# Kernel tuning notes

Measured on AMD Instinct MI355X. Metric: run time of the kernel, lower is better.

Reference implementation:

```python
import jax, jax.numpy as jnp
import numpy as np

B, D, V, T = 256, 1024, 32000, 64  # num_seqs, hidden dim, vocab, history len


def setup_inputs() -> dict:
    key = jax.random.key(0)
    ks = jax.random.split(key, 8)
    hidden = jax.random.normal(ks[0], (B, D), dtype=jnp.float32)
    embedding = jax.random.normal(ks[1], (V, D), dtype=jnp.float32) * (1.0 / np.sqrt(D))
    output_tokens = jax.random.randint(ks[2], (B, T), 0, V, dtype=jnp.int64)
    presence_penalties = jax.random.uniform(ks[3], (B,), dtype=jnp.float32)
    frequency_penalties = jax.random.uniform(ks[4], (B,), dtype=jnp.float32)
    temperatures = jax.random.uniform(ks[5], (B,), dtype=jnp.float32) + 0.5  # > eps
    top_ps = jax.random.uniform(ks[6], (B,), dtype=jnp.float32) * 0.5 + 0.5  # in [0.5, 1.0)
    top_ks = jax.random.randint(ks[7], (B,), 1, V, dtype=jnp.int64)
    return {
        "hidden": hidden,
        "embedding": embedding,
        "output_tokens": output_tokens,
        "presence_penalties": presence_penalties,
        "frequency_penalties": frequency_penalties,
        "temperatures": temperatures,
        "top_ps": top_ps,
        "top_ks": top_ks,
    }


def reference(hidden, embedding, output_tokens, presence_penalties,
              frequency_penalties, temperatures, top_ps, top_ks):
    # 1) logits = pruned hidden states @ embedding^T  -> [B, V]
    logits = jnp.einsum("bd,vd->bv", hidden, embedding)
    b, v = logits.shape

    # 2) presence/frequency penalties via per-row token histogram (np.bincount equiv)
    rows = jnp.broadcast_to(jnp.arange(b)[:, None], output_tokens.shape)
    counts = jnp.zeros((b, v), logits.dtype).at[rows, output_tokens].add(1.0)
    logits = logits - frequency_penalties[:, None] * counts \
                    - presence_penalties[:, None] * (counts > 0).astype(logits.dtype)

    # 3) temperature scaling
    logits = logits / temperatures[:, None]

    # 4) probabilities
    probs = jax.nn.softmax(logits, axis=-1)

    # 5) top-p / top-k: descending sort, cumsum masks, scatter back via inverse perm
    order = jnp.argsort(-probs, axis=-1)                       # descending order
    probs_sort = jnp.take_along_axis(probs, order, axis=-1)
    probs_cum = jnp.cumsum(probs_sort, axis=-1)
    top_p_mask = (probs_cum - probs_sort) > top_ps[:, None]
    top_k_mask = jnp.arange(v)[None, :] >= top_ks[:, None]
    probs_sort = jnp.where(top_p_mask | top_k_mask, 0.0, probs_sort)
    inv = jnp.argsort(order, axis=-1)
    filtered_probs = jnp.take_along_axis(probs_sort, inv, axis=-1)  # original order
    return filtered_probs
```

## Files before the change

### kernel.cpp

```cpp
#include <hip/hip_runtime.h>
#include <math.h>

#define NB 256
#define NV 32000
#define ND 1024
#define NT 64

#define GN 64
#define ASTR 56
#define NKB 64
#define ASLAB (256 * ASTR)
#define NGBLK (NV / GN)
#define INV2048F 4.8828125e-4f

#define NBIN 1024
#define HSTR 1032
#define HTOT (4 * HSTR)
#define FIX2 4294967296.0
#define SMASK ((1ull << 48) - 1ull)
#define SMEM_BYTES (NV * 4 + HTOT * 4)

typedef _Float16 f16x8 __attribute__((ext_vector_type(8)));
typedef _Float16 f16x4 __attribute__((ext_vector_type(4)));
typedef float f32x16 __attribute__((ext_vector_type(16)));
typedef __attribute__((address_space(3))) void lds_void;
typedef __attribute__((address_space(1))) void glb_void;

struct RowP2 {
  unsigned long long basePack;
  unsigned long long toppZfix;
  unsigned pfx;
  int ktop;
  float invZ;
  unsigned ustar;
  int m;
  int cEq;
};

__device__ __forceinline__ unsigned mono_enc(float f) {
  unsigned u = __float_as_uint(f);
  return (u & 0x80000000u) ? ~u : (u | 0x80000000u);
}
__device__ __forceinline__ float mono_dec(unsigned u) {
  return (u & 0x80000000u) ? __uint_as_float(u & 0x7FFFFFFFu) : __uint_as_float(~u);
}

__global__ __launch_bounds__(256) void convert_A(const float* __restrict__ hidden,
                                                 _Float16* __restrict__ A3) {
  const int kb = blockIdx.x, t = threadIdx.x;
  __shared__ _Float16 slab[ASLAB];
#pragma unroll
  for (int it = 0; it < 4; it++) {
    const int m = it * 64 + (t >> 2);
    const int k4 = (t & 3) * 4;
    float4 a4 = *(const float4*)(hidden + (size_t)m * ND + kb * 16 + k4);
    _Float16* base = slab + m * ASTR;
    float v[4] = {a4.x, a4.y, a4.z, a4.w};
#pragma unroll
    for (int q = 0; q < 4; q++) {
      const _Float16 h = (_Float16)v[q];
      const _Float16 l2 = (_Float16)((v[q] - (float)h) * 2048.0f);
      const int kk = k4 + q;
      base[kk] = h;
      base[16 + 2 * kk] = h;
      base[17 + 2 * kk] = l2;
    }
  }
  __syncthreads();
  const uint4* s = (const uint4*)slab;
  uint4* g = (uint4*)(A3 + (size_t)kb * ASLAB);
#pragma unroll
  for (int i = 0; i < 7; i++) g[i * 256 + t] = s[i * 256 + t];
}

__global__ __launch_bounds__(256, 2) void gemm_f16s(
    const float* __restrict__ Bm, const _Float16* __restrict__ A3,
    const float* __restrict__ temp, unsigned* __restrict__ rowmax,
    float* __restrict__ C) {
  __shared__ _Float16 Als[2][ASLAB];
  __shared__ _Float16 Bls[2][GN * ASTR];
  __shared__ float s_invT[256];
  __shared__ unsigned s_pm[256];

  const int t = threadIdx.x;
  const int l = t & 63, w = t >> 6;
  const int n0 = blockIdx.x * GN;
  s_invT[t] = 1.0f / temp[t];
  s_pm[t] = 0u;

  f32x16 accA[2][2] = {};
  f32x16 accB[2][2] = {};

  const int bn = t >> 2, bk4 = (t & 3) * 4;
  const int l31 = l & 31, lh = l >> 5;
  const int ka = lh * 8;
  const int mb = w * 64;

  const float* browp = Bm + (size_t)(n0 + bn) * ND + bk4;
  const char* gaBase = (const char*)A3 + (w * 7) * 1024 + l * 16;
  char* laB0 = (char*)&Als[0][0] + (w * 7) * 1024;
  char* laB1 = (char*)&Als[1][0] + (w * 7) * 1024;

#define ISSUE_A(kbn, LA)                                                        \
  do {                                                                          \
    const char* ga_ = gaBase + (size_t)(kbn) * (ASLAB * 2);                     \
    _Pragma("unroll") for (int i_ = 0; i_ < 7; i_++)                            \
        __builtin_amdgcn_global_load_lds((const glb_void*)(ga_ + i_ * 1024),    \
                                         (lds_void*)((LA) + i_ * 1024), 16, 0,  \
                                         0);                                    \
  } while (0)

#define BCONV(BV, DST)                                                          \
  do {                                                                          \
    const _Float16 h0_ = (_Float16)(BV).x, h1_ = (_Float16)(BV).y,              \
                   h2_ = (_Float16)(BV).z, h3_ = (_Float16)(BV).w;              \
    const _Float16 q0_ = (_Float16)(((BV).x - (float)h0_) * 2048.0f);           \
    const _Float16 q1_ = (_Float16)(((BV).y - (float)h1_) * 2048.0f);           \
    const _Float16 q2_ = (_Float16)(((BV).z - (float)h2_) * 2048.0f);           \
    const _Float16 q3_ = (_Float16)(((BV).w - (float)h3_) * 2048.0f);           \
    _Float16* prow_ = (DST) + bn * ASTR;                                        \
    *(f16x4*)(prow_ + bk4) = (f16x4){h0_, h1_, h2_, h3_};                       \
    *(f16x8*)(prow_ + 16 + 2 * bk4) =                                           \
        (f16x8){q0_, h0_, q1_, h1_, q2_, h2_, q3_, h3_};                        \
  } while (0)

#define COMPUTE(CUR)                                                                       \
  do {                                                                                     \
    const _Float16* Ap_ = &Als[CUR][0] + (size_t)(mb + l31) * ASTR + ka;                   \
    const _Float16* Bp_ = &Bls[CUR][0] + (size_t)l31 * ASTR + ka;                          \
    f16x8 a0_ = *(const f16x8*)(Ap_);                                                      \
    f16x8 a1_ = *(const f16x8*)(Ap_ + 32 * ASTR);                                          \
    f16x8 b0_ = *(const f16x8*)(Bp_);                                                      \
    f16x8 b1_ = *(const f16x8*)(Bp_ + 32 * ASTR);                                          \
    accA[0][0] = __builtin_amdgcn_mfma_f32_32x32x16_f16(a0_, b0_, accA[0][0], 0, 0, 0);    \
    accA[0][1] = __builtin_amdgcn_mfma_f32_32x32x16_f16(a0_, b1_, accA[0][1], 0, 0, 0);    \
    accA[1][0] = __builtin_amdgcn_mfma_f32_32x32x16_f16(a1_, b0_, accA[1][0], 0, 0, 0);    \
    accA[1][1] = __builtin_amdgcn_mfma_f32_32x32x16_f16(a1_, b1_, accA[1][1], 0, 0, 0);    \
    _Pragma("unroll") for (int s_ = 0; s_ < 2; s_++) {                                     \
      const int off_ = 16 + s_ * 16;                                                       \
      f16x8 c0_ = *(const f16x8*)(Ap_ + off_);                                             \
      f16x8 c1_ = *(const f16x8*)(Ap_ + 32 * ASTR + off_);                                 \
      f16x8 d0_ = *(const f16x8*)(Bp_ + off_);                                             \
      f16x8 d1_ = *(const f16x8*)(Bp_ + 32 * ASTR + off_);                                 \
      accB[0][0] = __builtin_amdgcn_mfma_f32_32x32x16_f16(c0_, d0_, accB[0][0], 0, 0, 0);  \
      accB[0][1] = __builtin_amdgcn_mfma_f32_32x32x16_f16(c0_, d1_, accB[0][1], 0, 0, 0);  \
      accB[1][0] = __builtin_amdgcn_mfma_f32_32x32x16_f16(c1_, d0_, accB[1][0], 0, 0, 0);  \
      accB[1][1] = __builtin_amdgcn_mfma_f32_32x32x16_f16(c1_, d1_, accB[1][1], 0, 0, 0);  \
    }                                                                                      \
  } while (0)

  ISSUE_A(0, laB0);
  __builtin_amdgcn_sched_barrier(0);
  float4 bv0 = *(const float4*)(browp);
  __builtin_amdgcn_sched_barrier(0);
  float4 bvA = *(const float4*)(browp + 16);
  __builtin_amdgcn_sched_barrier(0);
  asm volatile("s_waitcnt vmcnt(1)" ::: "memory");
  BCONV(bv0, &Bls[0][0]);
  asm volatile("s_waitcnt lgkmcnt(0)\ns_barrier" ::: "memory");

  float4 bvB;
  for (int kb = 0; kb < 62; kb += 2) {
    ISSUE_A(kb + 1, laB1);
    __builtin_amdgcn_sched_barrier(0);
    bvB = *(const float4*)(browp + (size_t)(kb + 2) * 16);
    __builtin_amdgcn_sched_barrier(0);
    asm volatile("s_waitcnt vmcnt(9)" ::: "memory");
    COMPUTE(0);
    __builtin_amdgcn_sched_barrier(0);
    asm volatile("s_waitcnt vmcnt(8)" ::: "memory");
    BCONV(bvA, &Bls[1][0]);
    asm volatile("s_waitcnt lgkmcnt(0)\ns_barrier" ::: "memory");

    ISSUE_A(kb + 2, laB0);
    __builtin_amdgcn_sched_barrier(0);
    bvA = *(const float4*)(browp + (size_t)(kb + 3) * 16);
    __builtin_amdgcn_sched_barrier(0);
    asm volatile("s_waitcnt vmcnt(9)" ::: "memory");
    COMPUTE(1);
    __builtin_amdgcn_sched_barrier(0);
    asm volatile("s_waitcnt vmcnt(8)" ::: "memory");
    BCONV(bvB, &Bls[0][0]);
    asm volatile("s_waitcnt lgkmcnt(0)\ns_barrier" ::: "memory");
  }

  ISSUE_A(63, laB1);
  __builtin_amdgcn_sched_barrier(0);
  asm volatile("s_waitcnt vmcnt(8)" ::: "memory");
  COMPUTE(0);
  __builtin_amdgcn_sched_barrier(0);
  asm volatile("s_waitcnt vmcnt(7)" ::: "memory");
  BCONV(bvA, &Bls[1][0]);
  asm volatile("s_waitcnt lgkmcnt(0)\ns_barrier" ::: "memory");

  asm volatile("s_waitcnt vmcnt(0)" ::: "memory");
  COMPUTE(1);

#undef ISSUE_A
#undef BCONV
#undef COMPUTE

#pragma unroll
  for (int mi = 0; mi < 2; mi++) {
#pragma unroll
    for (int r = 0; r < 16; r++) {
      const int row = mb + mi * 32 + (r & 3) + 8 * (r >> 2) + 4 * lh;
      const float it = s_invT[row];
      float v0 = (accA[mi][0][r] + accB[mi][0][r] * INV2048F) * it;
      float v1 = (accA[mi][1][r] + accB[mi][1][r] * INV2048F) * it;
      C[(size_t)row * NV + n0 + l31] = v0;
      C[(size_t)row * NV + n0 + 32 + l31] = v1;
      float mx = fmaxf(v0, v1);
#pragma unroll
      for (int o = 1; o < 32; o <<= 1) mx = fmaxf(mx, __shfl_xor(mx, o));
      if (l31 == 0) atomicMax(&s_pm[row], mono_enc(mx));
    }
  }
  __syncthreads();
  atomicMax(&rowmax[t], s_pm[t]);
}

__global__ __launch_bounds__(1024) void sample_row(
    float* __restrict__ buf, const unsigned* __restrict__ rowmax,
    const int* __restrict__ toks, const float* __restrict__ pres,
    const float* __restrict__ freq, const float* __restrict__ temp,
    const float* __restrict__ topp_a, const int* __restrict__ topk_a) {
  extern __shared__ char smem[];
  float* e = (float*)smem;
  unsigned* hist = (unsigned*)(smem + NV * 4);
  unsigned long long* suf = (unsigned long long*)hist;
  __shared__ int s_tok[NT];
  __shared__ int s_bs;
  __shared__ RowP2 sp;

  const int b = blockIdx.x, t = threadIdx.x;
  const int cp = (t >> 6) & 1;
  unsigned* loP = hist + cp * HSTR;
  unsigned* hcP = hist + 2 * HSTR + cp * HSTR;
  float* row = buf + (size_t)b * NV;

#define HACC(EV, BIN)                                                    \
  do {                                                                   \
    unsigned long long f_ = (unsigned long long)((double)(EV) * FIX2);   \
    unsigned flo_ = (unsigned)f_;                                        \
    unsigned old_ = atomicAdd(&loP[BIN], flo_);                          \
    unsigned hc_ = 0x10000u + (unsigned)(f_ >> 32) +                     \
                   ((old_ + flo_ < flo_) ? 1u : 0u);                     \
    atomicAdd(&hcP[BIN], hc_);                                           \
  } while (0)

  if (t < NT) s_tok[t] = toks[b * NT + t];
  for (int i = t; i < HTOT; i += 1024) hist[i] = 0u;
  for (int i4 = t; i4 < NV / 4; i4 += 1024)
    *(float4*)(e + i4 * 4) = *(const float4*)(row + i4 * 4);
  __syncthreads();

  if (t < NT) {
    const int tk = s_tok[t];
    bool first = true; int cnt = 0;
    for (int j = 0; j < NT; j++)
      if (s_tok[j] == tk) { if (j < t) first = false; cnt++; }
    if (first) e[tk] -= (freq[b] * (float)cnt + pres[b]) / temp[b];
  }
  __syncthreads();

  const float M = mono_dec(rowmax[b]);
  for (int i4 = t; i4 < NV / 4; i4 += 1024) {
    float4 x4 = *(const float4*)(e + i4 * 4);
    float4 e4;
    e4.x = expf(x4.x - M); e4.y = expf(x4.y - M);
    e4.z = expf(x4.z - M); e4.w = expf(x4.w - M);
    *(float4*)(e + i4 * 4) = e4;
    unsigned k;
    k = __float_as_uint(e4.x); if (k) HACC(e4.x, k >> 20);
    k = __float_as_uint(e4.y); if (k) HACC(e4.y, k >> 20);
    k = __float_as_uint(e4.z); if (k) HACC(e4.z, k >> 20);
    k = __float_as_uint(e4.w); if (k) HACC(e4.w, k >> 20);
  }
  __syncthreads();

  for (int level = 0; level < 3; level++) {
    const unsigned lo0 = hist[t], lo1 = hist[HSTR + t];
    const unsigned hc0 = hist[2 * HSTR + t], hc1 = hist[3 * HSTR + t];
    const unsigned c = (hc0 >> 16) + (hc1 >> 16);
    const unsigned long long sum =
        (((unsigned long long)((hc0 & 0xFFFFu) + (hc1 & 0xFFFFu))) << 32) +
        (unsigned long long)lo0 + (unsigned long long)lo1;
    const unsigned long long v = ((unsigned long long)c << 48) + sum;
    __syncthreads();
    suf[t] = v;
    __syncthreads();
    for (int off = 1; off < NBIN; off <<= 1) {
      unsigned long long add = (t + off < NBIN) ? suf[t + off] : 0ull;
      __syncthreads();
      suf[t] += add;
      __syncthreads();
    }
    const unsigned long long totalP = suf[0];
    if (t == 0) s_bs = NBIN - 1;
    __syncthreads();

    unsigned long long base, toppZ;
    int ktop_;
    if (level == 0) {
      ktop_ = topk_a[b];
      unsigned long long Zfix = totalP & SMASK;
      if (!Zfix) Zfix = 1ull;
      toppZ = (unsigned long long)((double)topp_a[b] * (double)Zfix);
      base = 0ull;
    } else {
      base = sp.basePack; toppZ = sp.toppZfix; ktop_ = sp.ktop;
    }

    {
      const unsigned long long sG = base + suf[t];
      const bool A = ((long long)(sG >> 48) < (long long)ktop_) && ((sG & SMASK) <= toppZ);
      const unsigned long long sP = base + ((t > 0) ? suf[t - 1] : totalP);
      const bool Ap = ((long long)(sP >> 48) < (long long)ktop_) && ((sP & SMASK) <= toppZ);
      if (A && !Ap) s_bs = t;
    }
    __syncthreads();
    if (t == 0) {
      const int bs = s_bs;
      const unsigned long long newBase = base + suf[bs];
      if (level == 0) {
        unsigned long long Zfix = totalP & SMASK;
        if (!Zfix) Zfix = 1ull;
        sp.invZ = (float)(FIX2 / (double)Zfix);
      }
      if (level < 2) {
        sp.basePack = newBase;
        sp.toppZfix = toppZ;
        sp.ktop = ktop_;
        sp.pfx = (level == 0) ? (unsigned)bs : ((sp.pfx << 10) | (unsigned)bs);
      } else {
        const unsigned ustar = (sp.pfx << 10) | (unsigned)bs;
        const unsigned long long raw = ((bs > 0) ? suf[bs - 1] : totalP) - suf[bs];
        const int cEq = (int)(raw >> 48);
        const long long Chi = (long long)(newBase >> 48);
        const unsigned long long Shi = newBase & SMASK;
        long long m = cEq;
        const long long lim = (long long)ktop_ - Chi;
        if (lim < m) m = lim;
        const double tf = (double)__uint_as_float(ustar) * FIX2;
        const double rem = (double)(toppZ - Shi);
        const double Rd = floor(rem / tf) + 1.0;
        if (Rd < (double)m) m = (long long)Rd;
        if (m < 1) m = 1;
        sp.ustar = ustar; sp.m = (int)m; sp.cEq = cEq;
      }
    }
    __syncthreads();

    if (level < 2) {
      for (int i = t; i < HTOT; i += 1024) hist[i] = 0u;
      __syncthreads();
      const unsigned pfx = sp.pfx;
      const int ms = (level == 0) ? 20 : 10;
      const int bsh = (level == 0) ? 10 : 0;
      for (int i4 = t; i4 < NV / 4; i4 += 1024) {
        float4 e4 = *(const float4*)(e + i4 * 4);
        unsigned k;
        k = __float_as_uint(e4.x); if (k && (k >> ms) == pfx) HACC(e4.x, (k >> bsh) & 1023u);
        k = __float_as_uint(e4.y); if (k && (k >> ms) == pfx) HACC(e4.y, (k >> bsh) & 1023u);
        k = __float_as_uint(e4.z); if (k && (k >> ms) == pfx) HACC(e4.z, (k >> bsh) & 1023u);
        k = __float_as_uint(e4.w); if (k && (k >> ms) == pfx) HACC(e4.w, (k >> bsh) & 1023u);
      }
      __syncthreads();
    }
  }
#undef HACC

  const unsigned ustar = sp.ustar;
  const float invZ = sp.invZ;
  if (sp.m >= sp.cEq) {
    for (int i4 = t; i4 < NV / 4; i4 += 1024) {
      float4 e4 = *(const float4*)(e + i4 * 4);
      float4 o4;
      unsigned k;
      k = __float_as_uint(e4.x); o4.x = (k >= ustar) ? e4.x * invZ : 0.f;
      k = __float_as_uint(e4.y); o4.y = (k >= ustar) ? e4.y * invZ : 0.f;
      k = __float_as_uint(e4.z); o4.z = (k >= ustar) ? e4.z * invZ : 0.f;
      k = __float_as_uint(e4.w); o4.w = (k >= ustar) ? e4.w * invZ : 0.f;
      *(float4*)(row + i4 * 4) = o4;
    }
  } else {
    const int m = sp.m;
    unsigned* rk = hist;
    const int base0 = t * 32;
    const int end0 = (base0 + 32 < NV) ? base0 + 32 : NV;
    int myc = 0;
    for (int v = base0; v < end0; v++)
      myc += (__float_as_uint(e[v]) == ustar);
    rk[t] = (unsigned)myc;
    __syncthreads();
    for (int off = 1; off < 1024; off <<= 1) {
      const unsigned a0 = rk[t];
      const unsigned an = (t >= off) ? rk[t - off] : 0u;
      __syncthreads();
      rk[t] = a0 + an;
      __syncthreads();
    }
    int r = (t > 0) ? (int)rk[t - 1] : 0;
    for (int v = base0; v < end0; v++) {
      const unsigned k = __float_as_uint(e[v]);
      float o = (k > ustar) ? e[v] * invZ : 0.f;
      if (k == ustar) { o = (r < m) ? e[v] * invZ : 0.f; r++; }
      row[v] = o;
    }
  }
}

extern "C" void kernel_launch(void* const* d_in, const int* in_sizes, int n_in,
                              void* d_out, int out_size, void* d_ws, size_t ws_size,
                              hipStream_t stream) {
  (void)in_sizes; (void)n_in; (void)out_size; (void)ws_size;
  const float* hidden = (const float*)d_in[0];
  const float* emb    = (const float*)d_in[1];
  const int*   toks   = (const int*)d_in[2];
  const float* pres   = (const float*)d_in[3];
  const float* freq   = (const float*)d_in[4];
  const float* temp   = (const float*)d_in[5];
  const float* topp   = (const float*)d_in[6];
  const int*   topk   = (const int*)d_in[7];
  float* out = (float*)d_out;

  const size_t offA3 = 0;
  const size_t offRM = 1835008;

  _Float16* A3 = (_Float16*)((char*)d_ws + offA3);
  unsigned* rowmax = (unsigned*)((char*)d_ws + offRM);

  hipFuncSetAttribute((const void*)sample_row,
                      hipFuncAttributeMaxDynamicSharedMemorySize, SMEM_BYTES);

  hipMemsetAsync((char*)d_ws + offRM, 0, 1024, stream);
  convert_A<<<NKB, 256, 0, stream>>>(hidden, A3);
  gemm_f16s<<<NGBLK, 256, 0, stream>>>(emb, A3, temp, rowmax, out);
  sample_row<<<NB, 1024, SMEM_BYTES, stream>>>(out, rowmax, toks, pres, freq,
                                               temp, topp, topk);
}
```

Measured before the change: 300.0 us.

## Widen GEMM N-tile to 128 columns, reusing each A fragment across four B tiles

Doubles the vocab tile per GEMM block from 64 to 128 columns. Each wave now computes 2x4 MFMA tiles per k-step, so every A fragment loaded from LDS feeds four B tiles, and the A slab is streamed from global memory half as often. B loading and fp16 hi/lo splitting are widened to 8 elements per thread, and the wait counts are adjusted. Occupancy drops to one block per CU with more accumulator registers, and only 250 blocks are launched, which may underfill the GPU.

```diff
diff --git a/kernel.cpp b/kernel.cpp
--- a/kernel.cpp
+++ b/kernel.cpp
@@ -6,7 +6,7 @@
 #define ND 1024
 #define NT 64
 
-#define GN 64
+#define GN 128
 #define ASTR 56
 #define NKB 64
 #define ASLAB (256 * ASTR)
@@ -73,7 +73,7 @@
   for (int i = 0; i < 7; i++) g[i * 256 + t] = s[i * 256 + t];
 }
 
-__global__ __launch_bounds__(256, 2) void gemm_f16s(
+__global__ __launch_bounds__(256, 1) void gemm_f16s(
     const float* __restrict__ Bm, const _Float16* __restrict__ A3,
     const float* __restrict__ temp, unsigned* __restrict__ rowmax,
     float* __restrict__ C) {
@@ -88,15 +88,15 @@
   s_invT[t] = 1.0f / temp[t];
   s_pm[t] = 0u;
 
-  f32x16 accA[2][2] = {};
-  f32x16 accB[2][2] = {};
-
-  const int bn = t >> 2, bk4 = (t & 3) * 4;
+  f32x16 accH[2][4] = {};
+  f32x16 accC[2][4] = {};
+
+  const int bn = t >> 1, k8 = (t & 1) * 8;
   const int l31 = l & 31, lh = l >> 5;
   const int ka = lh * 8;
   const int mb = w * 64;
 
-  const float* browp = Bm + (size_t)(n0 + bn) * ND + bk4;
+  const float* browp = Bm + (size_t)(n0 + bn) * ND + k8;
   const char* gaBase = (const char*)A3 + (w * 7) * 1024 + l * 16;
   char* laB0 = (char*)&Als[0][0] + (w * 7) * 1024;
   char* laB1 = (char*)&Als[1][0] + (w * 7) * 1024;
@@ -110,18 +110,22 @@
                                          0);                                    \
   } while (0)
 
-#define BCONV(BV, DST)                                                          \
+#define BCONV2(V0, V1, DST)                                                     \
   do {                                                                          \
-    const _Float16 h0_ = (_Float16)(BV).x, h1_ = (_Float16)(BV).y,              \
-                   h2_ = (_Float16)(BV).z, h3_ = (_Float16)(BV).w;              \
-    const _Float16 q0_ = (_Float16)(((BV).x - (float)h0_) * 2048.0f);           \
-    const _Float16 q1_ = (_Float16)(((BV).y - (float)h1_) * 2048.0f);           \
-    const _Float16 q2_ = (_Float16)(((BV).z - (float)h2_) * 2048.0f);           \
-    const _Float16 q3_ = (_Float16)(((BV).w - (float)h3_) * 2048.0f);           \
+    float vv_[8] = {(V0).x, (V0).y, (V0).z, (V0).w,                             \
+                    (V1).x, (V1).y, (V1).z, (V1).w};                            \
+    _Float16 h_[8], q_[8];                                                      \
+    _Pragma("unroll") for (int j_ = 0; j_ < 8; j_++) {                          \
+      h_[j_] = (_Float16)vv_[j_];                                               \
+      q_[j_] = (_Float16)((vv_[j_] - (float)h_[j_]) * 2048.0f);                 \
+    }                                                                           \
     _Float16* prow_ = (DST) + bn * ASTR;                                        \
-    *(f16x4*)(prow_ + bk4) = (f16x4){h0_, h1_, h2_, h3_};                       \
-    *(f16x8*)(prow_ + 16 + 2 * bk4) =                                           \
-        (f16x8){q0_, h0_, q1_, h1_, q2_, h2_, q3_, h3_};                        \
+    *(f16x8*)(prow_ + k8) =                                                     \
+        (f16x8){h_[0], h_[1], h_[2], h_[3], h_[4], h_[5], h_[6], h_[7]};        \
+    *(f16x8*)(prow_ + 16 + 2 * k8) =                                            \
+        (f16x8){q_[0], h_[0], q_[1], h_[1], q_[2], h_[2], q_[3], h_[3]};        \
+    *(f16x8*)(prow_ + 16 + 2 * k8 + 8) =                                        \
+        (f16x8){q_[4], h_[4], q_[5], h_[5], q_[6], h_[6], q_[7], h_[7]};        \
   } while (0)
 
 #define COMPUTE(CUR)                                                                       \
@@ -130,74 +134,76 @@
     const _Float16* Bp_ = &Bls[CUR][0] + (size_t)l31 * ASTR + ka;                          \
     f16x8 a0_ = *(const f16x8*)(Ap_);                                                      \
     f16x8 a1_ = *(const f16x8*)(Ap_ + 32 * ASTR);                                          \
-    f16x8 b0_ = *(const f16x8*)(Bp_);                                                      \
-    f16x8 b1_ = *(const f16x8*)(Bp_ + 32 * ASTR);                                          \
-    accA[0][0] = __builtin_amdgcn_mfma_f32_32x32x16_f16(a0_, b0_, accA[0][0], 0, 0, 0);    \
-    accA[0][1] = __builtin_amdgcn_mfma_f32_32x32x16_f16(a0_, b1_, accA[0][1], 0, 0, 0);    \
-    accA[1][0] = __builtin_amdgcn_mfma_f32_32x32x16_f16(a1_, b0_, accA[1][0], 0, 0, 0);    \
-    accA[1][1] = __builtin_amdgcn_mfma_f32_32x32x16_f16(a1_, b1_, accA[1][1], 0, 0, 0);    \
+    _Pragma("unroll") for (int nb_ = 0; nb_ < 4; nb_++) {                                  \
+      f16x8 b_ = *(const f16x8*)(Bp_ + nb_ * 32 * ASTR);                                   \
+      accH[0][nb_] = __builtin_amdgcn_mfma_f32_32x32x16_f16(a0_, b_, accH[0][nb_], 0,0,0); \
+      accH[1][nb_] = __builtin_amdgcn_mfma_f32_32x32x16_f16(a1_, b_, accH[1][nb_], 0,0,0); \
+    }                                                                                      \
     _Pragma("unroll") for (int s_ = 0; s_ < 2; s_++) {                                     \
       const int off_ = 16 + s_ * 16;                                                       \
       f16x8 c0_ = *(const f16x8*)(Ap_ + off_);                                             \
       f16x8 c1_ = *(const f16x8*)(Ap_ + 32 * ASTR + off_);                                 \
-      f16x8 d0_ = *(const f16x8*)(Bp_ + off_);                                             \
-      f16x8 d1_ = *(const f16x8*)(Bp_ + 32 * ASTR + off_);                                 \
-      accB[0][0] = __builtin_amdgcn_mfma_f32_32x32x16_f16(c0_, d0_, accB[0][0], 0, 0, 0);  \
-      accB[0][1] = __builtin_amdgcn_mfma_f32_32x32x16_f16(c0_, d1_, accB[0][1], 0, 0, 0);  \
-      accB[1][0] = __builtin_amdgcn_mfma_f32_32x32x16_f16(c1_, d0_, accB[1][0], 0, 0, 0);  \
-      accB[1][1] = __builtin_amdgcn_mfma_f32_32x32x16_f16(c1_, d1_, accB[1][1], 0, 0, 0);  \
+      _Pragma("unroll") for (int nb_ = 0; nb_ < 4; nb_++) {                                \
+        f16x8 d_ = *(const f16x8*)(Bp_ + nb_ * 32 * ASTR + off_);                          \
+        accC[0][nb_] = __builtin_amdgcn_mfma_f32_32x32x16_f16(c0_, d_, accC[0][nb_],0,0,0);\
+        accC[1][nb_] = __builtin_amdgcn_mfma_f32_32x32x16_f16(c1_, d_, accC[1][nb_],0,0,0);\
+      }                                                                                    \
     }                                                                                      \
   } while (0)
 
   ISSUE_A(0, laB0);
   __builtin_amdgcn_sched_barrier(0);
-  float4 bv0 = *(const float4*)(browp);
+  float4 b00 = *(const float4*)(browp);
+  float4 b01 = *(const float4*)(browp + 4);
   __builtin_amdgcn_sched_barrier(0);
-  float4 bvA = *(const float4*)(browp + 16);
+  float4 bA0 = *(const float4*)(browp + 16);
+  float4 bA1 = *(const float4*)(browp + 16 + 4);
   __builtin_amdgcn_sched_barrier(0);
-  asm volatile("s_waitcnt vmcnt(1)" ::: "memory");
-  BCONV(bv0, &Bls[0][0]);
+  asm volatile("s_waitcnt vmcnt(2)" ::: "memory");
+  BCONV2(b00, b01, &Bls[0][0]);
   asm volatile("s_waitcnt lgkmcnt(0)\ns_barrier" ::: "memory");
 
-  float4 bvB;
+  float4 bB0, bB1;
   for (int kb = 0; kb < 62; kb += 2) {
     ISSUE_A(kb + 1, laB1);
     __builtin_amdgcn_sched_barrier(0);
-    bvB = *(const float4*)(browp + (size_t)(kb + 2) * 16);
+    bB0 = *(const float4*)(browp + (size_t)(kb + 2) * 16);
+    bB1 = *(const float4*)(browp + (size_t)(kb + 2) * 16 + 4);
+    __builtin_amdgcn_sched_barrier(0);
+    asm volatile("s_waitcnt vmcnt(11)" ::: "memory");
+    COMPUTE(0);
     __builtin_amdgcn_sched_barrier(0);
     asm volatile("s_waitcnt vmcnt(9)" ::: "memory");
-    COMPUTE(0);
-    __builtin_amdgcn_sched_barrier(0);
-    asm volatile("s_waitcnt vmcnt(8)" ::: "memory");
-    BCONV(bvA, &Bls[1][0]);
+    BCONV2(bA0, bA1, &Bls[1][0]);
     asm volatile("s_waitcnt lgkmcnt(0)\ns_barrier" ::: "memory");
 
     ISSUE_A(kb + 2, laB0);
     __builtin_amdgcn_sched_barrier(0);
-    bvA = *(const float4*)(browp + (size_t)(kb + 3) * 16);
+    bA0 = *(const float4*)(browp + (size_t)(kb + 3) * 16);
+    bA1 = *(const float4*)(browp + (size_t)(kb + 3) * 16 + 4);
+    __builtin_amdgcn_sched_barrier(0);
+    asm volatile("s_waitcnt vmcnt(11)" ::: "memory");
+    COMPUTE(1);
     __builtin_amdgcn_sched_barrier(0);
     asm volatile("s_waitcnt vmcnt(9)" ::: "memory");
-    COMPUTE(1);
-    __builtin_amdgcn_sched_barrier(0);
-    asm volatile("s_waitcnt vmcnt(8)" ::: "memory");
-    BCONV(bvB, &Bls[0][0]);
+    BCONV2(bB0, bB1, &Bls[0][0]);
     asm volatile("s_waitcnt lgkmcnt(0)\ns_barrier" ::: "memory");
   }
 
   ISSUE_A(63, laB1);
   __builtin_amdgcn_sched_barrier(0);
-  asm volatile("s_waitcnt vmcnt(8)" ::: "memory");
+  asm volatile("s_waitcnt vmcnt(9)" ::: "memory");
   COMPUTE(0);
   __builtin_amdgcn_sched_barrier(0);
   asm volatile("s_waitcnt vmcnt(7)" ::: "memory");
-  BCONV(bvA, &Bls[1][0]);
+  BCONV2(bA0, bA1, &Bls[1][0]);
   asm volatile("s_waitcnt lgkmcnt(0)\ns_barrier" ::: "memory");
 
   asm volatile("s_waitcnt vmcnt(0)" ::: "memory");
   COMPUTE(1);
 
 #undef ISSUE_A
-#undef BCONV
+#undef BCONV2
 #undef COMPUTE
 
 #pragma unroll
@@ -206,11 +212,13 @@
     for (int r = 0; r < 16; r++) {
       const int row = mb + mi * 32 + (r & 3) + 8 * (r >> 2) + 4 * lh;
       const float it = s_invT[row];
-      float v0 = (accA[mi][0][r] + accB[mi][0][r] * INV2048F) * it;
-      float v1 = (accA[mi][1][r] + accB[mi][1][r] * INV2048F) * it;
-      C[(size_t)row * NV + n0 + l31] = v0;
-      C[(size_t)row * NV + n0 + 32 + l31] = v1;
-      float mx = fmaxf(v0, v1);
+      float mx = -3.4e38f;
+#pragma unroll
+      for (int nb = 0; nb < 4; nb++) {
+        const float v = (accH[mi][nb][r] + accC[mi][nb][r] * INV2048F) * it;
+        C[(size_t)row * NV + n0 + nb * 32 + l31] = v;
+        mx = fmaxf(mx, v);
+      }
 #pragma unroll
       for (int o = 1; o < 32; o <<= 1) mx = fmaxf(mx, __shfl_xor(mx, o));
       if (l31 == 0) atomicMax(&s_pm[row], mono_enc(mx));
```

Result: slower. 314.4 us (+4.8%).

## Shrink split-fp16 GEMM operand layout to hi+lo halves and regroup correction MFMAs

Applied to the files above, without the earlier changes.

The split-precision GEMM used a packed layout holding the hi half plus interleaved (lo,hi) pairs, giving 48 fp16 per row with a 56 stride. It now stores only hi and lo blocks of 16 each with a 40 stride. The correction term is computed as separate hi*lo and lo*hi MFMAs that share the hi operand loads. This cuts the A and B LDS footprint and the global-to-LDS traffic per k-step (5 instead of 7 loads per wave), with vmcnt waits adjusted to match. convert_A also becomes a simple per-thread store kernel over 256 blocks, with no LDS staging. The MFMA count per step stays at 12, so the gain comes from lower memory and LDS traffic, and the new stride may change LDS bank conflicts.

```diff
diff --git a/kernel.cpp b/kernel.cpp
--- a/kernel.cpp
+++ b/kernel.cpp
@@ -7,7 +7,7 @@
 #define NT 64
 
 #define GN 64
-#define ASTR 56
+#define ASTR 40
 #define NKB 64
 #define ASLAB (256 * ASTR)
 #define NGBLK (NV / GN)
@@ -47,30 +47,20 @@
 
 __global__ __launch_bounds__(256) void convert_A(const float* __restrict__ hidden,
                                                  _Float16* __restrict__ A3) {
-  const int kb = blockIdx.x, t = threadIdx.x;
-  __shared__ _Float16 slab[ASLAB];
+  const int g = blockIdx.x * 256 + threadIdx.x;
+  const int kb = g >> 10, rc = g & 1023, r = rc >> 2, c = rc & 3;
+  const float4 a4 = *(const float4*)(hidden + (size_t)r * ND + kb * 16 + c * 4);
+  const float v[4] = {a4.x, a4.y, a4.z, a4.w};
+  f16x4 h4, q4;
 #pragma unroll
-  for (int it = 0; it < 4; it++) {
-    const int m = it * 64 + (t >> 2);
-    const int k4 = (t & 3) * 4;
-    float4 a4 = *(const float4*)(hidden + (size_t)m * ND + kb * 16 + k4);
-    _Float16* base = slab + m * ASTR;
-    float v[4] = {a4.x, a4.y, a4.z, a4.w};
-#pragma unroll
-    for (int q = 0; q < 4; q++) {
-      const _Float16 h = (_Float16)v[q];
-      const _Float16 l2 = (_Float16)((v[q] - (float)h) * 2048.0f);
-      const int kk = k4 + q;
-      base[kk] = h;
-      base[16 + 2 * kk] = h;
-      base[17 + 2 * kk] = l2;
-    }
-  }
-  __syncthreads();
-  const uint4* s = (const uint4*)slab;
-  uint4* g = (uint4*)(A3 + (size_t)kb * ASLAB);
-#pragma unroll
-  for (int i = 0; i < 7; i++) g[i * 256 + t] = s[i * 256 + t];
+  for (int q = 0; q < 4; q++) {
+    const _Float16 h = (_Float16)v[q];
+    h4[q] = h;
+    q4[q] = (_Float16)((v[q] - (float)h) * 2048.0f);
+  }
+  _Float16* base = A3 + (size_t)kb * ASLAB + r * ASTR;
+  *(f16x4*)(base + c * 4) = h4;
+  *(f16x4*)(base + 16 + c * 4) = q4;
 }
 
 __global__ __launch_bounds__(256, 2) void gemm_f16s(
@@ -88,8 +78,8 @@
   s_invT[t] = 1.0f / temp[t];
   s_pm[t] = 0u;
 
-  f32x16 accA[2][2] = {};
-  f32x16 accB[2][2] = {};
+  f32x16 accH[2][2] = {};
+  f32x16 accC[2][2] = {};
 
   const int bn = t >> 2, bk4 = (t & 3) * 4;
   const int l31 = l & 31, lh = l >> 5;
@@ -97,14 +87,14 @@
   const int mb = w * 64;
 
   const float* browp = Bm + (size_t)(n0 + bn) * ND + bk4;
-  const char* gaBase = (const char*)A3 + (w * 7) * 1024 + l * 16;
-  char* laB0 = (char*)&Als[0][0] + (w * 7) * 1024;
-  char* laB1 = (char*)&Als[1][0] + (w * 7) * 1024;
+  const char* gaBase = (const char*)A3 + w * 5120 + l * 16;
+  char* laB0 = (char*)&Als[0][0] + w * 5120;
+  char* laB1 = (char*)&Als[1][0] + w * 5120;
 
 #define ISSUE_A(kbn, LA)                                                        \
   do {                                                                          \
     const char* ga_ = gaBase + (size_t)(kbn) * (ASLAB * 2);                     \
-    _Pragma("unroll") for (int i_ = 0; i_ < 7; i_++)                            \
+    _Pragma("unroll") for (int i_ = 0; i_ < 5; i_++)                            \
         __builtin_amdgcn_global_load_lds((const glb_void*)(ga_ + i_ * 1024),    \
                                          (lds_void*)((LA) + i_ * 1024), 16, 0,  \
                                          0);                                    \
@@ -112,41 +102,42 @@
 
 #define BCONV(BV, DST)                                                          \
   do {                                                                          \
-    const _Float16 h0_ = (_Float16)(BV).x, h1_ = (_Float16)(BV).y,              \
-                   h2_ = (_Float16)(BV).z, h3_ = (_Float16)(BV).w;              \
-    const _Float16 q0_ = (_Float16)(((BV).x - (float)h0_) * 2048.0f);           \
-    const _Float16 q1_ = (_Float16)(((BV).y - (float)h1_) * 2048.0f);           \
-    const _Float16 q2_ = (_Float16)(((BV).z - (float)h2_) * 2048.0f);           \
-    const _Float16 q3_ = (_Float16)(((BV).w - (float)h3_) * 2048.0f);           \
+    f16x4 h4_, q4_;                                                             \
+    const float vv_[4] = {(BV).x, (BV).y, (BV).z, (BV).w};                      \
+    _Pragma("unroll") for (int j_ = 0; j_ < 4; j_++) {                          \
+      const _Float16 h_ = (_Float16)vv_[j_];                                    \
+      h4_[j_] = h_;                                                             \
+      q4_[j_] = (_Float16)((vv_[j_] - (float)h_) * 2048.0f);                    \
+    }                                                                           \
     _Float16* prow_ = (DST) + bn * ASTR;                                        \
-    *(f16x4*)(prow_ + bk4) = (f16x4){h0_, h1_, h2_, h3_};                       \
-    *(f16x8*)(prow_ + 16 + 2 * bk4) =                                           \
-        (f16x8){q0_, h0_, q1_, h1_, q2_, h2_, q3_, h3_};                        \
+    *(f16x4*)(prow_ + bk4) = h4_;                                               \
+    *(f16x4*)(prow_ + 16 + bk4) = q4_;                                          \
   } while (0)
 
 #define COMPUTE(CUR)                                                                       \
   do {                                                                                     \
     const _Float16* Ap_ = &Als[CUR][0] + (size_t)(mb + l31) * ASTR + ka;                   \
     const _Float16* Bp_ = &Bls[CUR][0] + (size_t)l31 * ASTR + ka;                          \
-    f16x8 a0_ = *(const f16x8*)(Ap_);                                                      \
-    f16x8 a1_ = *(const f16x8*)(Ap_ + 32 * ASTR);                                          \
-    f16x8 b0_ = *(const f16x8*)(Bp_);                                                      \
-    f16x8 b1_ = *(const f16x8*)(Bp_ + 32 * ASTR);                                          \
-    accA[0][0] = __builtin_amdgcn_mfma_f32_32x32x16_f16(a0_, b0_, accA[0][0], 0, 0, 0);    \
-    accA[0][1] = __builtin_amdgcn_mfma_f32_32x32x16_f16(a0_, b1_, accA[0][1], 0, 0, 0);    \
-    accA[1][0] = __builtin_amdgcn_mfma_f32_32x32x16_f16(a1_, b0_, accA[1][0], 0, 0, 0);    \
-    accA[1][1] = __builtin_amdgcn_mfma_f32_32x32x16_f16(a1_, b1_, accA[1][1], 0, 0, 0);    \
-    _Pragma("unroll") for (int s_ = 0; s_ < 2; s_++) {                                     \
-      const int off_ = 16 + s_ * 16;                                                       \
-      f16x8 c0_ = *(const f16x8*)(Ap_ + off_);                                             \
-      f16x8 c1_ = *(const f16x8*)(Ap_ + 32 * ASTR + off_);                                 \
-      f16x8 d0_ = *(const f16x8*)(Bp_ + off_);                                             \
-      f16x8 d1_ = *(const f16x8*)(Bp_ + 32 * ASTR + off_);                                 \
-      accB[0][0] = __builtin_amdgcn_mfma_f32_32x32x16_f16(c0_, d0_, accB[0][0], 0, 0, 0);  \
-      accB[0][1] = __builtin_amdgcn_mfma_f32_32x32x16_f16(c0_, d1_, accB[0][1], 0, 0, 0);  \
-      accB[1][0] = __builtin_amdgcn_mfma_f32_32x32x16_f16(c1_, d0_, accB[1][0], 0, 0, 0);  \
-      accB[1][1] = __builtin_amdgcn_mfma_f32_32x32x16_f16(c1_, d1_, accB[1][1], 0, 0, 0);  \
-    }                                                                                      \
+    f16x8 a0h_ = *(const f16x8*)(Ap_);                                                     \
+    f16x8 a1h_ = *(const f16x8*)(Ap_ + 32 * ASTR);                                         \
+    f16x8 b0h_ = *(const f16x8*)(Bp_);                                                     \
+    f16x8 b1h_ = *(const f16x8*)(Bp_ + 32 * ASTR);                                         \
+    accH[0][0] = __builtin_amdgcn_mfma_f32_32x32x16_f16(a0h_, b0h_, accH[0][0], 0, 0, 0);  \
+    accH[0][1] = __builtin_amdgcn_mfma_f32_32x32x16_f16(a0h_, b1h_, accH[0][1], 0, 0, 0);  \
+    accH[1][0] = __builtin_amdgcn_mfma_f32_32x32x16_f16(a1h_, b0h_, accH[1][0], 0, 0, 0);  \
+    accH[1][1] = __builtin_amdgcn_mfma_f32_32x32x16_f16(a1h_, b1h_, accH[1][1], 0, 0, 0);  \
+    f16x8 b0q_ = *(const f16x8*)(Bp_ + 16);                                                \
+    f16x8 b1q_ = *(const f16x8*)(Bp_ + 32 * ASTR + 16);                                    \
+    accC[0][0] = __builtin_amdgcn_mfma_f32_32x32x16_f16(a0h_, b0q_, accC[0][0], 0, 0, 0);  \
+    accC[0][1] = __builtin_amdgcn_mfma_f32_32x32x16_f16(a0h_, b1q_, accC[0][1], 0, 0, 0);  \
+    accC[1][0] = __builtin_amdgcn_mfma_f32_32x32x16_f16(a1h_, b0q_, accC[1][0], 0, 0, 0);  \
+    accC[1][1] = __builtin_amdgcn_mfma_f32_32x32x16_f16(a1h_, b1q_, accC[1][1], 0, 0, 0);  \
+    f16x8 a0q_ = *(const f16x8*)(Ap_ + 16);                                                \
+    f16x8 a1q_ = *(const f16x8*)(Ap_ + 32 * ASTR + 16);                                    \
+    accC[0][0] = __builtin_amdgcn_mfma_f32_32x32x16_f16(a0q_, b0h_, accC[0][0], 0, 0, 0);  \
+    accC[0][1] = __builtin_amdgcn_mfma_f32_32x32x16_f16(a0q_, b1h_, accC[0][1], 0, 0, 0);  \
+    accC[1][0] = __builtin_amdgcn_mfma_f32_32x32x16_f16(a1q_, b0h_, accC[1][0], 0, 0, 0);  \
+    accC[1][1] = __builtin_amdgcn_mfma_f32_32x32x16_f16(a1q_, b1h_, accC[1][1], 0, 0, 0);  \
   } while (0)
 
   ISSUE_A(0, laB0);
@@ -165,10 +156,10 @@
     __builtin_amdgcn_sched_barrier(0);
     bvB = *(const float4*)(browp + (size_t)(kb + 2) * 16);
     __builtin_amdgcn_sched_barrier(0);
-    asm volatile("s_waitcnt vmcnt(9)" ::: "memory");
+    asm volatile("s_waitcnt vmcnt(7)" ::: "memory");
     COMPUTE(0);
     __builtin_amdgcn_sched_barrier(0);
-    asm volatile("s_waitcnt vmcnt(8)" ::: "memory");
+    asm volatile("s_waitcnt vmcnt(6)" ::: "memory");
     BCONV(bvA, &Bls[1][0]);
     asm volatile("s_waitcnt lgkmcnt(0)\ns_barrier" ::: "memory");
 
@@ -176,20 +167,20 @@
     __builtin_amdgcn_sched_barrier(0);
     bvA = *(const float4*)(browp + (size_t)(kb + 3) * 16);
     __builtin_amdgcn_sched_barrier(0);
-    asm volatile("s_waitcnt vmcnt(9)" ::: "memory");
+    asm volatile("s_waitcnt vmcnt(7)" ::: "memory");
     COMPUTE(1);
     __builtin_amdgcn_sched_barrier(0);
-    asm volatile("s_waitcnt vmcnt(8)" ::: "memory");
+    asm volatile("s_waitcnt vmcnt(6)" ::: "memory");
     BCONV(bvB, &Bls[0][0]);
     asm volatile("s_waitcnt lgkmcnt(0)\ns_barrier" ::: "memory");
   }
 
   ISSUE_A(63, laB1);
   __builtin_amdgcn_sched_barrier(0);
-  asm volatile("s_waitcnt vmcnt(8)" ::: "memory");
+  asm volatile("s_waitcnt vmcnt(6)" ::: "memory");
   COMPUTE(0);
   __builtin_amdgcn_sched_barrier(0);
-  asm volatile("s_waitcnt vmcnt(7)" ::: "memory");
+  asm volatile("s_waitcnt vmcnt(5)" ::: "memory");
   BCONV(bvA, &Bls[1][0]);
   asm volatile("s_waitcnt lgkmcnt(0)\ns_barrier" ::: "memory");
 
@@ -206,8 +197,8 @@
     for (int r = 0; r < 16; r++) {
       const int row = mb + mi * 32 + (r & 3) + 8 * (r >> 2) + 4 * lh;
       const float it = s_invT[row];
-      float v0 = (accA[mi][0][r] + accB[mi][0][r] * INV2048F) * it;
-      float v1 = (accA[mi][1][r] + accB[mi][1][r] * INV2048F) * it;
+      float v0 = (accH[mi][0][r] + accC[mi][0][r] * INV2048F) * it;
+      float v1 = (accH[mi][1][r] + accC[mi][1][r] * INV2048F) * it;
       C[(size_t)row * NV + n0 + l31] = v0;
       C[(size_t)row * NV + n0 + 32 + l31] = v1;
       float mx = fmaxf(v0, v1);
@@ -426,7 +417,7 @@
   float* out = (float*)d_out;
 
   const size_t offA3 = 0;
-  const size_t offRM = 1835008;
+  const size_t offRM = 1310720;
 
   _Float16* A3 = (_Float16*)((char*)d_ws + offA3);
   unsigned* rowmax = (unsigned*)((char*)d_ws + offRM);
@@ -435,7 +426,7 @@
                       hipFuncAttributeMaxDynamicSharedMemorySize, SMEM_BYTES);
 
   hipMemsetAsync((char*)d_ws + offRM, 0, 1024, stream);
-  convert_A<<<NKB, 256, 0, stream>>>(hidden, A3);
+  convert_A<<<256, 256, 0, stream>>>(hidden, A3);
   gemm_f16s<<<NGBLK, 256, 0, stream>>>(emb, A3, temp, rowmax, out);
   sample_row<<<NB, 1024, SMEM_BYTES, stream>>>(out, rowmax, toks, pres, freq,
                                                temp, topp, topk);
```

Result: faster. 292.0 us (-2.7%).
